# Performance work log

Hardware: AMD Instinct MI355X
Metric: run time of the kernel (lower is better)

The kernel has to match this reference:

```python
import jax, jax.numpy as jnp
import numpy as np

NEG_SLOPE = 0.2  # PyG GATConv default negative_slope
BN_EPS = 1e-5


def gat_layer(x, src, dst, W, b, a_src, a_dst, heads, out_ch, concat):
    # x: [N, Fin]; W: [Fin, heads*out_ch]; a_src/a_dst: [heads, out_ch]
    N = x.shape[0]
    h = (x @ W).reshape(N, heads, out_ch)
    s = (h * a_src).sum(-1)            # [N, H]
    d = (h * a_dst).sum(-1)            # [N, H]
    e = jax.nn.leaky_relu(s[src] + d[dst], NEG_SLOPE)   # [E, H]
    # segment softmax over incoming edges of each destination node
    m = jax.ops.segment_max(e, dst, num_segments=N)
    ex = jnp.exp(e - m[dst])
    denom = jax.ops.segment_sum(ex, dst, num_segments=N)
    alpha = ex / (denom[dst] + 1e-16)                   # [E, H]
    out = jax.ops.segment_sum(alpha[:, :, None] * h[src], dst, num_segments=N)  # [N,H,C]
    out = out.reshape(N, heads * out_ch) if concat else out.mean(axis=1)
    return out + b


def batchnorm(x, gamma, beta):
    mu = x.mean(axis=0)
    var = x.var(axis=0)
    return gamma * (x - mu) * jax.lax.rsqrt(var + BN_EPS) + beta


def setup_inputs() -> dict:
    key = jax.random.key(0)
    ks = jax.random.split(key, 24)
    N, E, Fin, Hd, heads, C = 50000, 800000, 128, 64, 4, 2
    wdim = Hd * heads  # 256
    inp = {
        'x': jax.random.normal(ks[0], (N, Fin), jnp.float32),
        'edge_index': jax.random.randint(ks[1], (2, E), 0, N, jnp.int64),
    }
    def glorot(k, shape):
        fan = shape[0] + shape[-1]
        return jax.random.normal(k, shape, jnp.float32) * np.sqrt(2.0 / fan)
    # layer 0: Fin -> heads x Hd (concat)
    inp['W0'] = glorot(ks[2], (Fin, wdim)); inp['b0'] = jnp.zeros((wdim,), jnp.float32)
    inp['asrc0'] = glorot(ks[3], (heads, Hd)); inp['adst0'] = glorot(ks[4], (heads, Hd))
    inp['g0'] = jnp.ones((wdim,), jnp.float32); inp['be0'] = jnp.zeros((wdim,), jnp.float32)
    # layer 1: wdim -> heads x Hd (concat)
    inp['W1'] = glorot(ks[5], (wdim, wdim)); inp['b1'] = jnp.zeros((wdim,), jnp.float32)
    inp['asrc1'] = glorot(ks[6], (heads, Hd)); inp['adst1'] = glorot(ks[7], (heads, Hd))
    inp['g1'] = jnp.ones((wdim,), jnp.float32); inp['be1'] = jnp.zeros((wdim,), jnp.float32)
    # layer 2: wdim -> 1 head x Hd (no concat)
    inp['W2'] = glorot(ks[8], (wdim, Hd)); inp['b2'] = jnp.zeros((Hd,), jnp.float32)
    inp['asrc2'] = glorot(ks[9], (1, Hd)); inp['adst2'] = glorot(ks[10], (1, Hd))
    inp['g2'] = jnp.ones((Hd,), jnp.float32); inp['be2'] = jnp.zeros((Hd,), jnp.float32)
    # classifier: Linear(2*Hd, Hd) -> ReLU -> Linear(Hd, C)
    inp['Wc1'] = glorot(ks[11], (2 * Hd, Hd)); inp['bc1'] = jnp.zeros((Hd,), jnp.float32)
    inp['Wc2'] = glorot(ks[12], (Hd, C)); inp['bc2'] = jnp.zeros((C,), jnp.float32)
    return inp


def reference(x, edge_index, W0, b0, asrc0, adst0, g0, be0,
              W1, b1, asrc1, adst1, g1, be1,
              W2, b2, asrc2, adst2, g2, be2,
              Wc1, bc1, Wc2, bc2):
    N = x.shape[0]
    # add self-loops (PyG GATConv default)
    loops = jnp.arange(N, dtype=edge_index.dtype)
    src = jnp.concatenate([edge_index[0], loops])
    dst = jnp.concatenate([edge_index[1], loops])
    heads, Hd = asrc0.shape[0], asrc0.shape[1]

    h = gat_layer(x, src, dst, W0, b0, asrc0, adst0, heads, Hd, True)
    h = jax.nn.relu(batchnorm(h, g0, be0))
    h = gat_layer(h, src, dst, W1, b1, asrc1, adst1, heads, Hd, True)
    h = jax.nn.relu(batchnorm(h, g1, be1))
    h = gat_layer(h, src, dst, W2, b2, asrc2, adst2, 1, Hd, False)
    h = jax.nn.relu(batchnorm(h, g2, be2))

    pooled = jnp.concatenate([h.mean(axis=0, keepdims=True),
                              h.max(axis=0, keepdims=True)], axis=1)  # [1, 2*Hd]
    z = jax.nn.relu(pooled @ Wc1 + bc1)
    return z @ Wc2 + bc2  # [1, num_classes]
```

## Files before the change

### kernel.cpp

```cpp
#include <hip/hip_runtime.h>


typedef unsigned int uint;
typedef unsigned short ushort;

#define NEG_SLOPE 0.2f
#define BN_EPS 1e-5f
#define NB_RED 256

__device__ __forceinline__ float bf2f(uint u) { return __uint_as_float(u << 16); }
__device__ __forceinline__ ushort f2bf(float f) {
    uint u = __float_as_uint(f);
    u += 0x7fff + ((u >> 16) & 1);
    return (ushort)(u >> 16);
}
__device__ __forceinline__ float lrelu(float x) { return x > 0.f ? x : NEG_SLOPE * x; }


__global__ void prep_kernel(const float* __restrict__ x, ushort* __restrict__ xb,
                            int total_real, int total_pad,
                            const float* __restrict__ W0, ushort* __restrict__ w0t,
                            const float* __restrict__ W1, ushort* __restrict__ w1t,
                            const float* __restrict__ W2, ushort* __restrict__ w2t,
                            const int* __restrict__ ei, int* __restrict__ deg, int E) {
    int i = blockIdx.x * blockDim.x + threadIdx.x;
    if (i < total_pad) {
        xb[i] = (i < total_real) ? f2bf(x[i]) : (ushort)0;
        return;
    }
    int j = i - total_pad;
    if (j < 32768) {
        int n = j / 128, k = j - n * 128;
        w0t[j] = f2bf(W0[(size_t)k * 256 + n]);
        return;
    }
    j -= 32768;
    if (j < 65536) {
        int n = j / 256, k = j - n * 256;
        w1t[j] = f2bf(W1[(size_t)k * 256 + n]);
        return;
    }
    j -= 65536;
    if (j < 16384) {
        int n = j / 256, k = j - n * 256;
        w2t[j] = f2bf(W2[(size_t)k * 64 + n]);
        return;
    }
    j -= 16384;
    if (j < E) atomicAdd(&deg[ei[E + j]], 1);
}


__global__ void scan_part(const int* __restrict__ deg, int* __restrict__ offsets,
                          int* __restrict__ bsum, int N) {
    __shared__ int sh[256];
    int t = threadIdx.x;
    int base = blockIdx.x * 1024 + t * 4;
    int v0 = (base + 0 < N) ? deg[base + 0] : 0;
    int v1 = (base + 1 < N) ? deg[base + 1] : 0;
    int v2 = (base + 2 < N) ? deg[base + 2] : 0;
    int v3 = (base + 3 < N) ? deg[base + 3] : 0;
    int s = v0 + v1 + v2 + v3;
    sh[t] = s;
    __syncthreads();
    for (int off = 1; off < 256; off <<= 1) {
        int y = (t >= off) ? sh[t - off] : 0;
        __syncthreads();
        sh[t] += y;
        __syncthreads();
    }
    int p = sh[t] - s;
    if (base + 0 < N) offsets[base + 0] = p;
    p += v0;
    if (base + 1 < N) offsets[base + 1] = p;
    p += v1;
    if (base + 2 < N) offsets[base + 2] = p;
    p += v2;
    if (base + 3 < N) offsets[base + 3] = p;
    if (t == 255) bsum[blockIdx.x] = sh[255];
}

__global__ void scan_top(const int* __restrict__ bsum, int* __restrict__ bexcl,
                         int nb, int* __restrict__ offsets, int N) {
    if (threadIdx.x == 0) {
        int run = 0;
        for (int b = 0; b < nb; ++b) { bexcl[b] = run; run += bsum[b]; }
        offsets[N] = run;
    }
}

__global__ void scan_add(int* __restrict__ offsets, int* __restrict__ cursor,
                         const int* __restrict__ bexcl, int N) {
    int add = bexcl[blockIdx.x];
    int base = blockIdx.x * 1024 + threadIdx.x * 4;
#pragma unroll
    for (int k = 0; k < 4; ++k) {
        int i = base + k;
        if (i < N) { int v = offsets[i] + add; offsets[i] = v; cursor[i] = v; }
    }
}

__global__ void scatter_kernel(const int* __restrict__ ei, int* __restrict__ cursor,
                               int* __restrict__ srcs, int E) {
    int e = blockIdx.x * blockDim.x + threadIdx.x;
    if (e < E) {
        int s = ei[e];
        int d = ei[E + e];
        int p = atomicAdd(&cursor[d], 1);
        srcs[p] = s;
    }
}


typedef __attribute__((ext_vector_type(8))) short bf16x8;
typedef __attribute__((ext_vector_type(4))) float floatx4;

template <int BN, int H>
__launch_bounds__(256)
__global__ void mfma_gemm_bt(const ushort* __restrict__ A, const ushort* __restrict__ Bt,
                             ushort* __restrict__ C, const float* __restrict__ asrc,
                             const float* __restrict__ adst, float* __restrict__ sv,
                             float* __restrict__ dv, int K, int Nn) {
    constexpr int WCOLS = (BN == 128) ? 2 : 1;
    constexpr int WROWS = 4 / WCOLS;
    constexpr int MT = 128 / (WROWS * 16);
    constexpr int NT = BN / (WCOLS * 16);
    constexpr int BCALLS = (BN * 32 * 2) / 4096;

    __shared__ ushort As[128 * 32];
    __shared__ ushort Bs[BN * 32];

    int t = threadIdx.x;
    int w = t >> 6, l = t & 63;
    int row0 = blockIdx.x * 128;
    int col0 = blockIdx.y * BN;
    int wr = (w / WCOLS) * (MT * 16);
    int wc = (w % WCOLS) * (NT * 16);

    floatx4 acc[MT][NT];
#pragma unroll
    for (int mi = 0; mi < MT; ++mi)
#pragma unroll
        for (int ni = 0; ni < NT; ++ni)
#pragma unroll
            for (int r = 0; r < 4; ++r) acc[mi][ni][r] = 0.f;

    int mrow = l & 15;
    int kc = (l >> 4) * 8;

    for (int kt = 0; kt < K; kt += 32) {
#pragma unroll
        for (int c = 0; c < 2; ++c) {
            int idx = c * 256 + t;
            const ushort* gp = A + (size_t)(row0 + (idx >> 2)) * K + kt + (idx & 3) * 8;
            __builtin_amdgcn_global_load_lds(
                (const __attribute__((address_space(1))) void*)gp,
                (__attribute__((address_space(3))) void*)(As + (idx & ~63) * 8),
                16, 0, 0);
        }
#pragma unroll
        for (int c = 0; c < BCALLS; ++c) {
            int idx = c * 256 + t;
            const ushort* gp = Bt + (size_t)(col0 + (idx >> 2)) * K + kt + (idx & 3) * 8;
            __builtin_amdgcn_global_load_lds(
                (const __attribute__((address_space(1))) void*)gp,
                (__attribute__((address_space(3))) void*)(Bs + (idx & ~63) * 8),
                16, 0, 0);
        }
        __syncthreads();

        bf16x8 af[MT], bfr[NT];
#pragma unroll
        for (int mi = 0; mi < MT; ++mi)
            af[mi] = *(const bf16x8*)&As[(wr + mi * 16 + mrow) * 32 + kc];
#pragma unroll
        for (int ni = 0; ni < NT; ++ni)
            bfr[ni] = *(const bf16x8*)&Bs[(wc + ni * 16 + mrow) * 32 + kc];
#pragma unroll
        for (int mi = 0; mi < MT; ++mi)
#pragma unroll
            for (int ni = 0; ni < NT; ++ni)
                acc[mi][ni] = __builtin_amdgcn_mfma_f32_16x16x32_bf16(
                    af[mi], bfr[ni], acc[mi][ni], 0, 0, 0);
        __syncthreads();
    }

#pragma unroll
    for (int mi = 0; mi < MT; ++mi) {
        int rbase = row0 + wr + mi * 16 + (l >> 4) * 4;
#pragma unroll
        for (int ni = 0; ni < NT; ++ni) {
            int col = col0 + wc + ni * 16 + (l & 15);
#pragma unroll
            for (int r = 0; r < 4; ++r)
                C[(size_t)(rbase + r) * Nn + col] = f2bf(acc[mi][ni][r]);
        }
    }

    float av[NT], bv[NT];
#pragma unroll
    for (int ni = 0; ni < NT; ++ni) {
        int ch = col0 + wc + ni * 16 + (l & 15);
        av[ni] = asrc[ch];
        bv[ni] = adst[ch];
    }
    int gh = (col0 + wc) >> 6;
#pragma unroll
    for (int mi = 0; mi < MT; ++mi) {
#pragma unroll
        for (int r = 0; r < 4; ++r) {
            float s = 0.f, d = 0.f;
#pragma unroll
            for (int ni = 0; ni < NT; ++ni) {
                float hv = acc[mi][ni][r];
                s += hv * av[ni];
                d += hv * bv[ni];
            }
#pragma unroll
            for (int m = 8; m >= 1; m >>= 1) {
                s += __shfl_xor(s, m);
                d += __shfl_xor(d, m);
            }
            if ((l & 15) == 0) {
                int row = row0 + wr + mi * 16 + (l >> 4) * 4 + r;
                sv[row * H + gh] = s;
                dv[row * H + gh] = d;
            }
        }
    }
}


__launch_bounds__(128)
__global__ void agg4_kernel(const ushort* __restrict__ hb, const float* __restrict__ sv,
                            const float* __restrict__ dv, const int* __restrict__ offsets,
                            const int* __restrict__ srcs, const float* __restrict__ bias,
                            ushort* __restrict__ zb, int N) {
    __shared__ float lsum[4][256];
    __shared__ float lden[4][4];

    int i = blockIdx.x;
    int t = threadIdx.x;
    int grp = t >> 5, gl = t & 31;
    int head = gl >> 3;
    int beg = offsets[i], end = offsets[i + 1];

    float d_i = dv[i * 4 + head];
    float ax[8] = {};
    float den = 0.f;

    int j = beg + grp;
    int srcn = (j < end) ? srcs[j] : 0;
    while (j < end) {
        float sval = sv[srcn * 4 + head];
        uint4 q = *(const uint4*)&hb[(size_t)srcn * 256 + gl * 8];
        int jn = j + 4;
        int srcn_n = (jn < end) ? srcs[jn] : 0;
        float wgt = __expf(fminf(lrelu(sval + d_i), 60.f));
        den += wgt;
        uint pr[4] = {q.x, q.y, q.z, q.w};
#pragma unroll
        for (int k = 0; k < 4; ++k) {
            ax[2 * k]     += wgt * bf2f(pr[k] & 0xffffu);
            ax[2 * k + 1] += wgt * bf2f(pr[k] >> 16);
        }
        j = jn; srcn = srcn_n;
    }

#pragma unroll
    for (int k = 0; k < 8; ++k) lsum[grp][gl * 8 + k] = ax[k];
    if ((gl & 7) == 0) lden[grp][head] = den;
    __syncthreads();

    int h = t >> 5;
    float wself = __expf(fminf(lrelu(sv[i * 4 + h] + dv[i * 4 + h]), 60.f));
    float dtot = lden[0][h] + lden[1][h] + lden[2][h] + lden[3][h] + wself + 1e-16f;
    float rden = 1.f / dtot;
    uint p = *(const uint*)&hb[(size_t)i * 256 + 2 * t];
    float a0 = lsum[0][2 * t] + lsum[1][2 * t] + lsum[2][2 * t] + lsum[3][2 * t]
             + wself * bf2f(p & 0xffffu);
    float a1 = lsum[0][2 * t + 1] + lsum[1][2 * t + 1] + lsum[2][2 * t + 1]
             + lsum[3][2 * t + 1] + wself * bf2f(p >> 16);
    a0 = a0 * rden + bias[2 * t];
    a1 = a1 * rden + bias[2 * t + 1];
    *(uint*)&zb[(size_t)i * 256 + 2 * t] = (uint)f2bf(a0) | ((uint)f2bf(a1) << 16);
}


__launch_bounds__(64)
__global__ void agg1_kernel(const ushort* __restrict__ hb, const float* __restrict__ sv,
                            const float* __restrict__ dv, const int* __restrict__ offsets,
                            const int* __restrict__ srcs, const float* __restrict__ bias,
                            ushort* __restrict__ zb, int N) {
    int i = blockIdx.x;
    int l = threadIdx.x;
    int grp = l >> 4, gl = l & 15;
    int beg = offsets[i], end = offsets[i + 1];

    float d_i = dv[i];
    float ax[4] = {};
    float den = 0.f;

    int j = beg + grp;
    int srcn = (j < end) ? srcs[j] : 0;
    while (j < end) {
        float sval = sv[srcn];
        uint2 q = *(const uint2*)&hb[(size_t)srcn * 64 + gl * 4];
        int jn = j + 4;
        int srcn_n = (jn < end) ? srcs[jn] : 0;
        float wgt = __expf(fminf(lrelu(sval + d_i), 60.f));
        den += wgt;
        ax[0] += wgt * bf2f(q.x & 0xffffu);
        ax[1] += wgt * bf2f(q.x >> 16);
        ax[2] += wgt * bf2f(q.y & 0xffffu);
        ax[3] += wgt * bf2f(q.y >> 16);
        j = jn; srcn = srcn_n;
    }

#pragma unroll
    for (int k = 0; k < 4; ++k) {
        ax[k] += __shfl_xor(ax[k], 16);
        ax[k] += __shfl_xor(ax[k], 32);
    }
    den += __shfl_xor(den, 16);
    den += __shfl_xor(den, 32);

    if (l < 16) {
        float wself = __expf(fminf(lrelu(sv[i] + d_i), 60.f));
        float rden = 1.f / (den + wself + 1e-16f);
        uint2 q = *(const uint2*)&hb[(size_t)i * 64 + gl * 4];
        float a0 = (ax[0] + wself * bf2f(q.x & 0xffffu)) * rden + bias[gl * 4 + 0];
        float a1 = (ax[1] + wself * bf2f(q.x >> 16)) * rden + bias[gl * 4 + 1];
        float a2 = (ax[2] + wself * bf2f(q.y & 0xffffu)) * rden + bias[gl * 4 + 2];
        float a3 = (ax[3] + wself * bf2f(q.y >> 16)) * rden + bias[gl * 4 + 3];
        uint2 o;
        o.x = (uint)f2bf(a0) | ((uint)f2bf(a1) << 16);
        o.y = (uint)f2bf(a2) | ((uint)f2bf(a3) << 16);
        *(uint2*)&zb[(size_t)i * 64 + gl * 4] = o;
    }
}


template <int F>
__launch_bounds__(256)
__global__ void bn_stats_kernel(const ushort* __restrict__ x, float* __restrict__ ps,
                                float* __restrict__ pq, int N) {
    constexpr int OCT = F / 8;
    __shared__ float lds_s[F], lds_q[F];
    int t = threadIdx.x;
    if (t < F) { lds_s[t] = 0.f; lds_q[t] = 0.f; }
    __syncthreads();

    float s[8] = {}, q[8] = {};
    int total8 = N * F / 8;
    for (int idx = blockIdx.x * 256 + t; idx < total8; idx += NB_RED * 256) {
        uint4 v = ((const uint4*)x)[idx];
        uint pr[4] = {v.x, v.y, v.z, v.w};
#pragma unroll
        for (int k = 0; k < 4; ++k) {
            float a = bf2f(pr[k] & 0xffffu);
            float b = bf2f(pr[k] >> 16);
            s[2 * k] += a;     q[2 * k] += a * a;
            s[2 * k + 1] += b; q[2 * k + 1] += b * b;
        }
    }
    int co = t % OCT;
#pragma unroll
    for (int j = 0; j < 8; ++j) {
        atomicAdd(&lds_s[co * 8 + j], s[j]);
        atomicAdd(&lds_q[co * 8 + j], q[j]);
    }
    __syncthreads();
    if (t < F) {
        ps[blockIdx.x * F + t] = lds_s[t];
        pq[blockIdx.x * F + t] = lds_q[t];
    }
}

__global__ void bn_final_kernel(const float* __restrict__ ps, const float* __restrict__ pq,
                                const float* __restrict__ g, const float* __restrict__ be,
                                float* __restrict__ scale, float* __restrict__ shift,
                                int N, int F) {
    int t = threadIdx.x;
    if (t < F) {
        float s = 0.f, q = 0.f;
        for (int b = 0; b < NB_RED; ++b) { s += ps[b * F + t]; q += pq[b * F + t]; }
        float mean = s / (float)N;
        float var = q / (float)N - mean * mean;
        float sc = g[t] * rsqrtf(var + BN_EPS);
        scale[t] = sc;
        shift[t] = be[t] - sc * mean;
    }
}

__global__ void bn_apply_kernel(uint* __restrict__ x, const float* __restrict__ scale,
                                const float* __restrict__ shift, int totalPairs, int Fmask) {
    int i = blockIdx.x * blockDim.x + threadIdx.x;
    if (i < totalPairs) {
        uint p = x[i];
        int c0 = (2 * i) & Fmask;
        float v0 = fmaxf(bf2f(p & 0xffffu) * scale[c0] + shift[c0], 0.f);
        float v1 = fmaxf(bf2f(p >> 16) * scale[c0 + 1] + shift[c0 + 1], 0.f);
        x[i] = (uint)f2bf(v0) | ((uint)f2bf(v1) << 16);
    }
}


__launch_bounds__(256)
__global__ void pool_kernel(const ushort* __restrict__ y, const float* __restrict__ scale,
                            const float* __restrict__ shift, float* __restrict__ psum,
                            float* __restrict__ pmax, int N) {
    constexpr int F = 64, OCT = 8;
    __shared__ float lds_s[F];
    __shared__ uint lds_m[F];
    int t = threadIdx.x;
    if (t < F) { lds_s[t] = 0.f; lds_m[t] = 0u; }
    __syncthreads();

    int co = t % OCT;
    float sc[8], sh[8];
#pragma unroll
    for (int j = 0; j < 8; ++j) { sc[j] = scale[co * 8 + j]; sh[j] = shift[co * 8 + j]; }

    float s[8] = {}, m[8] = {};
    int total8 = N * F / 8;
    for (int idx = blockIdx.x * 256 + t; idx < total8; idx += NB_RED * 256) {
        uint4 v = ((const uint4*)y)[idx];
        uint pr[4] = {v.x, v.y, v.z, v.w};
#pragma unroll
        for (int k = 0; k < 4; ++k) {
            float a = fmaxf(bf2f(pr[k] & 0xffffu) * sc[2 * k] + sh[2 * k], 0.f);
            float b = fmaxf(bf2f(pr[k] >> 16) * sc[2 * k + 1] + sh[2 * k + 1], 0.f);
            s[2 * k] += a;     m[2 * k] = fmaxf(m[2 * k], a);
            s[2 * k + 1] += b; m[2 * k + 1] = fmaxf(m[2 * k + 1], b);
        }
    }
#pragma unroll
    for (int j = 0; j < 8; ++j) {
        atomicAdd(&lds_s[co * 8 + j], s[j]);
        atomicMax(&lds_m[co * 8 + j], __float_as_uint(m[j]));
    }
    __syncthreads();
    if (t < F) {
        psum[blockIdx.x * F + t] = lds_s[t];
        pmax[blockIdx.x * F + t] = __uint_as_float(lds_m[t]);
    }
}

__global__ void classify_kernel(const float* __restrict__ psum, const float* __restrict__ pmax,
                                const float* __restrict__ Wc1, const float* __restrict__ bc1,
                                const float* __restrict__ Wc2, const float* __restrict__ bc2,
                                float* __restrict__ out, int N) {
    __shared__ float pooled[128];
    __shared__ float z[64];
    int t = threadIdx.x;
    if (t < 64) {
        float s = 0.f;
        for (int b = 0; b < NB_RED; ++b) s += psum[b * 64 + t];
        pooled[t] = s / (float)N;
    } else {
        int c = t - 64;
        float m = 0.f;
        for (int b = 0; b < NB_RED; ++b) m = fmaxf(m, pmax[b * 64 + c]);
        pooled[t] = m;
    }
    __syncthreads();
    if (t < 64) {
        float a = bc1[t];
        for (int k = 0; k < 128; ++k) a += pooled[k] * Wc1[k * 64 + t];
        z[t] = a > 0.f ? a : 0.f;
    }
    __syncthreads();
    if (t < 2) {
        float a = bc2[t];
        for (int j = 0; j < 64; ++j) a += z[j] * Wc2[j * 2 + t];
        out[t] = a;
    }
}


extern "C" void kernel_launch(void* const* d_in, const int* in_sizes, int n_in,
                              void* d_out, int out_size, void* d_ws, size_t ws_size,
                              hipStream_t stream) {
    const float* x   = (const float*)d_in[0];
    const int*   ei  = (const int*)d_in[1];
    const float* W0  = (const float*)d_in[2];  const float* b0  = (const float*)d_in[3];
    const float* as0 = (const float*)d_in[4];  const float* ad0 = (const float*)d_in[5];
    const float* g0  = (const float*)d_in[6];  const float* be0 = (const float*)d_in[7];
    const float* W1  = (const float*)d_in[8];  const float* b1  = (const float*)d_in[9];
    const float* as1 = (const float*)d_in[10]; const float* ad1 = (const float*)d_in[11];
    const float* g1  = (const float*)d_in[12]; const float* be1 = (const float*)d_in[13];
    const float* W2  = (const float*)d_in[14]; const float* b2  = (const float*)d_in[15];
    const float* as2 = (const float*)d_in[16]; const float* ad2 = (const float*)d_in[17];
    const float* g2  = (const float*)d_in[18]; const float* be2 = (const float*)d_in[19];
    const float* Wc1 = (const float*)d_in[20]; const float* bc1 = (const float*)d_in[21];
    const float* Wc2 = (const float*)d_in[22]; const float* bc2 = (const float*)d_in[23];
    float* out = (float*)d_out;

    const int N = in_sizes[0] / 128;
    const int E = in_sizes[1] / 2;
    const int Mpad = ((N + 127) / 128) * 128;
    const int NB_SCAN = (N + 1023) / 1024;

    char* ws = (char*)d_ws;
    size_t o = 0;
    auto alloc = [&](size_t bytes) -> void* {
        void* p = ws + o;
        o = (o + bytes + 255) & ~(size_t)255;
        return p;
    };
    int*    deg     = (int*)alloc((size_t)N * 4);
    int*    offsets = (int*)alloc((size_t)(N + 1) * 4);
    int*    cursor  = (int*)alloc((size_t)N * 4);
    int*    srcs    = (int*)alloc((size_t)E * 4);
    int*    bsum    = (int*)alloc((size_t)NB_SCAN * 4);
    int*    bexcl   = (int*)alloc((size_t)NB_SCAN * 4);
    ushort* xb      = (ushort*)alloc((size_t)Mpad * 128 * 2);
    ushort* w0t     = (ushort*)alloc((size_t)256 * 128 * 2);
    ushort* w1t     = (ushort*)alloc((size_t)256 * 256 * 2);
    ushort* w2t     = (ushort*)alloc((size_t)64 * 256 * 2);
    ushort* hb      = (ushort*)alloc((size_t)Mpad * 256 * 2);
    ushort* zb      = (ushort*)alloc((size_t)Mpad * 256 * 2);
    float*  sv      = (float*)alloc((size_t)Mpad * 4 * 4);
    float*  dv      = (float*)alloc((size_t)Mpad * 4 * 4);
    float*  ps      = (float*)alloc((size_t)NB_RED * 256 * 4);
    float*  pq      = (float*)alloc((size_t)NB_RED * 256 * 4);
    float*  scale   = (float*)alloc(256 * 4);
    float*  shift   = (float*)alloc(256 * 4);
    float*  psum    = (float*)alloc((size_t)NB_RED * 64 * 4);
    float*  pmax    = (float*)alloc((size_t)NB_RED * 64 * 4);

    hipMemsetAsync(deg, 0, (size_t)N * 4, stream);
    int prep_total = Mpad * 128 + 32768 + 65536 + 16384 + E;
    prep_kernel<<<(prep_total + 255) / 256, 256, 0, stream>>>(
        x, xb, N * 128, Mpad * 128, W0, w0t, W1, w1t, W2, w2t, ei, deg, E);

    scan_part<<<NB_SCAN, 256, 0, stream>>>(deg, offsets, bsum, N);
    scan_top<<<1, 64, 0, stream>>>(bsum, bexcl, NB_SCAN, offsets, N);
    scan_add<<<NB_SCAN, 256, 0, stream>>>(offsets, cursor, bexcl, N);
    scatter_kernel<<<(E + 255) / 256, 256, 0, stream>>>(ei, cursor, srcs, E);

    {
        dim3 gg(Mpad / 128, 2);
        mfma_gemm_bt<128, 4><<<gg, 256, 0, stream>>>(xb, w0t, hb, as0, ad0, sv, dv, 128, 256);
        agg4_kernel<<<N, 128, 0, stream>>>(hb, sv, dv, offsets, srcs, b0, zb, N);
        bn_stats_kernel<256><<<NB_RED, 256, 0, stream>>>(zb, ps, pq, N);
        bn_final_kernel<<<1, 256, 0, stream>>>(ps, pq, g0, be0, scale, shift, N, 256);
        bn_apply_kernel<<<(N * 128 + 255) / 256, 256, 0, stream>>>((uint*)zb, scale, shift,
                                                                   N * 128, 255);
    }
    {
        dim3 gg(Mpad / 128, 2);
        mfma_gemm_bt<128, 4><<<gg, 256, 0, stream>>>(zb, w1t, hb, as1, ad1, sv, dv, 256, 256);
        agg4_kernel<<<N, 128, 0, stream>>>(hb, sv, dv, offsets, srcs, b1, zb, N);
        bn_stats_kernel<256><<<NB_RED, 256, 0, stream>>>(zb, ps, pq, N);
        bn_final_kernel<<<1, 256, 0, stream>>>(ps, pq, g1, be1, scale, shift, N, 256);
        bn_apply_kernel<<<(N * 128 + 255) / 256, 256, 0, stream>>>((uint*)zb, scale, shift,
                                                                   N * 128, 255);
    }
    {
        dim3 gg(Mpad / 128, 1);
        mfma_gemm_bt<64, 1><<<gg, 256, 0, stream>>>(zb, w2t, hb, as2, ad2, sv, dv, 256, 64);
        agg1_kernel<<<N, 64, 0, stream>>>(hb, sv, dv, offsets, srcs, b2, zb, N);
        bn_stats_kernel<64><<<NB_RED, 256, 0, stream>>>(zb, ps, pq, N);
        bn_final_kernel<<<1, 64, 0, stream>>>(ps, pq, g2, be2, scale, shift, N, 64);
    }

    pool_kernel<<<NB_RED, 256, 0, stream>>>(zb, scale, shift, psum, pmax, N);
    classify_kernel<<<1, 128, 0, stream>>>(psum, pmax, Wc1, bc1, Wc2, bc2, out, N);
}
```

Measured before the change: 593.7 us.

## Double-buffer neighbor gathers in aggregation, pack FMAs, pad LDS, swizzle GEMM blocks

The aggregation kernels now keep two edges' gathers in flight ahead of use, so more loads are outstanding per lane and gather latency can overlap with the exp/FMA work. Accumulation uses 2-wide float vectors so the compiler can emit packed FMAs, and leaky-ReLU becomes a branchless fmax. The agg4 shared-memory reduction buffer is padded to cut LDS bank conflicts. The GEMM launch becomes a 1D grid remapped so the two column blocks of a row group run close together, which may improve L2 reuse of the A tile. The cost is higher register pressure in the aggregation kernels and more index arithmetic.

```diff
diff --git a/kernel.cpp b/kernel.cpp
--- a/kernel.cpp
+++ b/kernel.cpp
@@ -7,6 +7,8 @@
 #define NEG_SLOPE 0.2f
 #define BN_EPS 1e-5f
 #define NB_RED 256
+
+typedef __attribute__((ext_vector_type(2))) float f32x2;
 
 __device__ __forceinline__ float bf2f(uint u) { return __uint_as_float(u << 16); }
 __device__ __forceinline__ ushort f2bf(float f) {
@@ -14,7 +16,7 @@
     u += 0x7fff + ((u >> 16) & 1);
     return (ushort)(u >> 16);
 }
-__device__ __forceinline__ float lrelu(float x) { return x > 0.f ? x : NEG_SLOPE * x; }
+__device__ __forceinline__ float lrelu(float x) { return fmaxf(x, NEG_SLOPE * x); }
 
 
 __global__ void prep_kernel(const float* __restrict__ x, ushort* __restrict__ xb,
@@ -132,8 +134,27 @@
 
     int t = threadIdx.x;
     int w = t >> 6, l = t & 63;
-    int row0 = blockIdx.x * 128;
-    int col0 = blockIdx.y * BN;
+
+    int rb, cb;
+    if (BN == 128) {
+        int nbr = (int)gridDim.x >> 1;
+        int full = (nbr & ~7) << 1;
+        int id = blockIdx.x;
+        if (id < full) {
+            rb = ((id >> 4) << 3) + (id & 7);
+            cb = (id >> 3) & 1;
+        } else {
+            int o = id - full;
+            int rem = nbr & 7;
+            rb = (nbr & ~7) + (rem ? (o % rem) : 0);
+            cb = rem ? (o / rem) : 0;
+        }
+    } else {
+        rb = blockIdx.x;
+        cb = 0;
+    }
+    int row0 = rb * 128;
+    int col0 = cb * BN;
     int wr = (w / WCOLS) * (MT * 16);
     int wc = (w % WCOLS) * (NT * 16);
 
@@ -231,12 +252,25 @@
 }
 
 
+#define ACCUM4(q, s) { \
+    float e_ = (s) + d_i; \
+    float w_ = __expf(fminf(fmaxf(e_, NEG_SLOPE * e_), 60.f)); \
+    den += w_; \
+    f32x2 wv_ = {w_, w_}; \
+    uint pr_[4] = {(q).x, (q).y, (q).z, (q).w}; \
+    _Pragma("unroll") \
+    for (int k_ = 0; k_ < 4; ++k_) { \
+        f32x2 hv_ = {__uint_as_float(pr_[k_] << 16), \
+                     __uint_as_float(pr_[k_] & 0xffff0000u)}; \
+        ax[k_] += wv_ * hv_; \
+    } }
+
 __launch_bounds__(128)
 __global__ void agg4_kernel(const ushort* __restrict__ hb, const float* __restrict__ sv,
                             const float* __restrict__ dv, const int* __restrict__ offsets,
                             const int* __restrict__ srcs, const float* __restrict__ bias,
                             ushort* __restrict__ zb, int N) {
-    __shared__ float lsum[4][256];
+    __shared__ float lsum[4][288];
     __shared__ float lden[4][4];
 
     int i = blockIdx.x;
@@ -246,46 +280,81 @@
     int beg = offsets[i], end = offsets[i + 1];
 
     float d_i = dv[i * 4 + head];
-    float ax[8] = {};
+    f32x2 ax[4] = {};
     float den = 0.f;
 
+    const ushort* hrow = hb + gl * 8;
+
     int j = beg + grp;
-    int srcn = (j < end) ? srcs[j] : 0;
-    while (j < end) {
-        float sval = sv[srcn * 4 + head];
-        uint4 q = *(const uint4*)&hb[(size_t)srcn * 256 + gl * 8];
-        int jn = j + 4;
-        int srcn_n = (jn < end) ? srcs[jn] : 0;
-        float wgt = __expf(fminf(lrelu(sval + d_i), 60.f));
-        den += wgt;
-        uint pr[4] = {q.x, q.y, q.z, q.w};
-#pragma unroll
-        for (int k = 0; k < 4; ++k) {
-            ax[2 * k]     += wgt * bf2f(pr[k] & 0xffffu);
-            ax[2 * k + 1] += wgt * bf2f(pr[k] >> 16);
-        }
-        j = jn; srcn = srcn_n;
-    }
-
-#pragma unroll
-    for (int k = 0; k < 8; ++k) lsum[grp][gl * 8 + k] = ax[k];
+    float sA = 0.f, sB = 0.f;
+    uint4 qA = {0, 0, 0, 0}, qB = {0, 0, 0, 0};
+    if (j < end) {
+        int n = srcs[j];
+        sA = sv[n * 4 + head];
+        qA = *(const uint4*)(hrow + (size_t)n * 256);
+    }
+    if (j + 4 < end) {
+        int n = srcs[j + 4];
+        sB = sv[n * 4 + head];
+        qB = *(const uint4*)(hrow + (size_t)n * 256);
+    }
+
+    while (j + 4 < end) {
+        int jc = j + 8, jd = j + 12;
+        float sC = 0.f, sD = 0.f;
+        uint4 qC = {0, 0, 0, 0}, qD = {0, 0, 0, 0};
+        if (jc < end) {
+            int n = srcs[jc];
+            sC = sv[n * 4 + head];
+            qC = *(const uint4*)(hrow + (size_t)n * 256);
+        }
+        if (jd < end) {
+            int n = srcs[jd];
+            sD = sv[n * 4 + head];
+            qD = *(const uint4*)(hrow + (size_t)n * 256);
+        }
+        ACCUM4(qA, sA);
+        ACCUM4(qB, sB);
+        sA = sC; qA = qC;
+        sB = sD; qB = qD;
+        j += 8;
+    }
+    if (j < end) ACCUM4(qA, sA);
+
+#pragma unroll
+    for (int k = 0; k < 4; ++k) {
+        lsum[grp][gl * 9 + 2 * k]     = ax[k].x;
+        lsum[grp][gl * 9 + 2 * k + 1] = ax[k].y;
+    }
     if ((gl & 7) == 0) lden[grp][head] = den;
     __syncthreads();
 
     int h = t >> 5;
-    float wself = __expf(fminf(lrelu(sv[i * 4 + h] + dv[i * 4 + h]), 60.f));
+    float e_self = sv[i * 4 + h] + dv[i * 4 + h];
+    float wself = __expf(fminf(fmaxf(e_self, NEG_SLOPE * e_self), 60.f));
     float dtot = lden[0][h] + lden[1][h] + lden[2][h] + lden[3][h] + wself + 1e-16f;
     float rden = 1.f / dtot;
+    int idx = 2 * t + (t >> 2);
     uint p = *(const uint*)&hb[(size_t)i * 256 + 2 * t];
-    float a0 = lsum[0][2 * t] + lsum[1][2 * t] + lsum[2][2 * t] + lsum[3][2 * t]
-             + wself * bf2f(p & 0xffffu);
-    float a1 = lsum[0][2 * t + 1] + lsum[1][2 * t + 1] + lsum[2][2 * t + 1]
-             + lsum[3][2 * t + 1] + wself * bf2f(p >> 16);
+    float a0 = lsum[0][idx] + lsum[1][idx] + lsum[2][idx] + lsum[3][idx]
+             + wself * __uint_as_float(p << 16);
+    float a1 = lsum[0][idx + 1] + lsum[1][idx + 1] + lsum[2][idx + 1]
+             + lsum[3][idx + 1] + wself * __uint_as_float(p & 0xffff0000u);
     a0 = a0 * rden + bias[2 * t];
     a1 = a1 * rden + bias[2 * t + 1];
     *(uint*)&zb[(size_t)i * 256 + 2 * t] = (uint)f2bf(a0) | ((uint)f2bf(a1) << 16);
 }
 
+
+#define ACCUM1(q, s) { \
+    float e_ = (s) + d_i; \
+    float w_ = __expf(fminf(fmaxf(e_, NEG_SLOPE * e_), 60.f)); \
+    den += w_; \
+    f32x2 wv_ = {w_, w_}; \
+    f32x2 h0_ = {__uint_as_float((q).x << 16), __uint_as_float((q).x & 0xffff0000u)}; \
+    f32x2 h1_ = {__uint_as_float((q).y << 16), __uint_as_float((q).y & 0xffff0000u)}; \
+    ax[0] += wv_ * h0_; \
+    ax[1] += wv_ * h1_; }
 
 __launch_bounds__(64)
 __global__ void agg1_kernel(const ushort* __restrict__ hb, const float* __restrict__ sv,
@@ -298,41 +367,65 @@
     int beg = offsets[i], end = offsets[i + 1];
 
     float d_i = dv[i];
-    float ax[4] = {};
+    f32x2 ax[2] = {};
     float den = 0.f;
 
+    const ushort* hrow = hb + gl * 4;
+
     int j = beg + grp;
-    int srcn = (j < end) ? srcs[j] : 0;
-    while (j < end) {
-        float sval = sv[srcn];
-        uint2 q = *(const uint2*)&hb[(size_t)srcn * 64 + gl * 4];
-        int jn = j + 4;
-        int srcn_n = (jn < end) ? srcs[jn] : 0;
-        float wgt = __expf(fminf(lrelu(sval + d_i), 60.f));
-        den += wgt;
-        ax[0] += wgt * bf2f(q.x & 0xffffu);
-        ax[1] += wgt * bf2f(q.x >> 16);
-        ax[2] += wgt * bf2f(q.y & 0xffffu);
-        ax[3] += wgt * bf2f(q.y >> 16);
-        j = jn; srcn = srcn_n;
-    }
-
+    float sA = 0.f, sB = 0.f;
+    uint2 qA = {0, 0}, qB = {0, 0};
+    if (j < end) {
+        int n = srcs[j];
+        sA = sv[n];
+        qA = *(const uint2*)(hrow + (size_t)n * 64);
+    }
+    if (j + 4 < end) {
+        int n = srcs[j + 4];
+        sB = sv[n];
+        qB = *(const uint2*)(hrow + (size_t)n * 64);
+    }
+
+    while (j + 4 < end) {
+        int jc = j + 8, jd = j + 12;
+        float sC = 0.f, sD = 0.f;
+        uint2 qC = {0, 0}, qD = {0, 0};
+        if (jc < end) {
+            int n = srcs[jc];
+            sC = sv[n];
+            qC = *(const uint2*)(hrow + (size_t)n * 64);
+        }
+        if (jd < end) {
+            int n = srcs[jd];
+            sD = sv[n];
+            qD = *(const uint2*)(hrow + (size_t)n * 64);
+        }
+        ACCUM1(qA, sA);
+        ACCUM1(qB, sB);
+        sA = sC; qA = qC;
+        sB = sD; qB = qD;
+        j += 8;
+    }
+    if (j < end) ACCUM1(qA, sA);
+
+    float a4[4] = {ax[0].x, ax[0].y, ax[1].x, ax[1].y};
 #pragma unroll
     for (int k = 0; k < 4; ++k) {
-        ax[k] += __shfl_xor(ax[k], 16);
-        ax[k] += __shfl_xor(ax[k], 32);
+        a4[k] += __shfl_xor(a4[k], 16);
+        a4[k] += __shfl_xor(a4[k], 32);
     }
     den += __shfl_xor(den, 16);
     den += __shfl_xor(den, 32);
 
     if (l < 16) {
-        float wself = __expf(fminf(lrelu(sv[i] + d_i), 60.f));
+        float e_self = sv[i] + d_i;
+        float wself = __expf(fminf(fmaxf(e_self, NEG_SLOPE * e_self), 60.f));
         float rden = 1.f / (den + wself + 1e-16f);
         uint2 q = *(const uint2*)&hb[(size_t)i * 64 + gl * 4];
-        float a0 = (ax[0] + wself * bf2f(q.x & 0xffffu)) * rden + bias[gl * 4 + 0];
-        float a1 = (ax[1] + wself * bf2f(q.x >> 16)) * rden + bias[gl * 4 + 1];
-        float a2 = (ax[2] + wself * bf2f(q.y & 0xffffu)) * rden + bias[gl * 4 + 2];
-        float a3 = (ax[3] + wself * bf2f(q.y >> 16)) * rden + bias[gl * 4 + 3];
+        float a0 = (a4[0] + wself * bf2f(q.x & 0xffffu)) * rden + bias[gl * 4 + 0];
+        float a1 = (a4[1] + wself * bf2f(q.x >> 16)) * rden + bias[gl * 4 + 1];
+        float a2 = (a4[2] + wself * bf2f(q.y & 0xffffu)) * rden + bias[gl * 4 + 2];
+        float a3 = (a4[3] + wself * bf2f(q.y >> 16)) * rden + bias[gl * 4 + 3];
         uint2 o;
         o.x = (uint)f2bf(a0) | ((uint)f2bf(a1) << 16);
         o.y = (uint)f2bf(a2) | ((uint)f2bf(a3) << 16);
@@ -501,6 +594,7 @@
     const int E = in_sizes[1] / 2;
     const int Mpad = ((N + 127) / 128) * 128;
     const int NB_SCAN = (N + 1023) / 1024;
+    const int NBROW = Mpad / 128;
 
     char* ws = (char*)d_ws;
     size_t o = 0;
@@ -541,8 +635,7 @@
     scatter_kernel<<<(E + 255) / 256, 256, 0, stream>>>(ei, cursor, srcs, E);
 
     {
-        dim3 gg(Mpad / 128, 2);
-        mfma_gemm_bt<128, 4><<<gg, 256, 0, stream>>>(xb, w0t, hb, as0, ad0, sv, dv, 128, 256);
+        mfma_gemm_bt<128, 4><<<NBROW * 2, 256, 0, stream>>>(xb, w0t, hb, as0, ad0, sv, dv, 128, 256);
         agg4_kernel<<<N, 128, 0, stream>>>(hb, sv, dv, offsets, srcs, b0, zb, N);
         bn_stats_kernel<256><<<NB_RED, 256, 0, stream>>>(zb, ps, pq, N);
         bn_final_kernel<<<1, 256, 0, stream>>>(ps, pq, g0, be0, scale, shift, N, 256);
@@ -550,8 +643,7 @@
                                                                    N * 128, 255);
     }
     {
-        dim3 gg(Mpad / 128, 2);
-        mfma_gemm_bt<128, 4><<<gg, 256, 0, stream>>>(zb, w1t, hb, as1, ad1, sv, dv, 256, 256);
+        mfma_gemm_bt<128, 4><<<NBROW * 2, 256, 0, stream>>>(zb, w1t, hb, as1, ad1, sv, dv, 256, 256);
         agg4_kernel<<<N, 128, 0, stream>>>(hb, sv, dv, offsets, srcs, b1, zb, N);
         bn_stats_kernel<256><<<NB_RED, 256, 0, stream>>>(zb, ps, pq, N);
         bn_final_kernel<<<1, 256, 0, stream>>>(ps, pq, g1, be1, scale, shift, N, 256);
@@ -559,8 +651,7 @@
                                                                    N * 128, 255);
     }
     {
-        dim3 gg(Mpad / 128, 1);
-        mfma_gemm_bt<64, 1><<<gg, 256, 0, stream>>>(zb, w2t, hb, as2, ad2, sv, dv, 256, 64);
+        mfma_gemm_bt<64, 1><<<NBROW, 256, 0, stream>>>(zb, w2t, hb, as2, ad2, sv, dv, 256, 64);
         agg1_kernel<<<N, 64, 0, stream>>>(hb, sv, dv, offsets, srcs, b2, zb, N);
         bn_stats_kernel<64><<<NB_RED, 256, 0, stream>>>(zb, ps, pq, N);
         bn_final_kernel<<<1, 64, 0, stream>>>(ps, pq, g2, be2, scale, shift, N, 64);
```

New measurement: 585.0 us. About the same (-1.5%).
